# Performance work log

Measured on AMD Instinct MI355X. Metric: run time of the kernel, lower is better.

The kernel has to match this reference:

```python
import jax, jax.numpy as jnp
import numpy as np
from jax import lax

L = 12        # transformer layers
H = 768       # d_model
NH = 12       # heads
HD = H // NH  # head dim
F = 2048      # ffn dim (torch TransformerEncoderLayer default)
V = 128       # vocab_size (level logits)
NLV = 128     # n_levels (rows of routed weight W)
B, S = 8, 512
EPS = 1e-5


def _layer_norm(x, g, b):
    mu = jnp.mean(x, axis=-1, keepdims=True)
    var = jnp.mean(jnp.square(x - mu), axis=-1, keepdims=True)
    return g * (x - mu) / jnp.sqrt(var + EPS) + b


def _encoder(x, layer_params):
    # torch nn.TransformerEncoderLayer, post-LN, ReLU, eval mode (no dropout)
    def block(h, p):
        Wqkv, bqkv, Wo, bo, g1, bb1, W1, b1f, W2, b2f, g2, bb2 = p
        qkv = h @ Wqkv.T + bqkv                      # [B,S,3H]
        q, k, v = jnp.split(qkv, 3, axis=-1)
        sh = (h.shape[0], h.shape[1], NH, HD)
        q, k, v = q.reshape(sh), k.reshape(sh), v.reshape(sh)
        scores = jnp.einsum('bqhd,bkhd->bhqk', q, k) / jnp.sqrt(jnp.asarray(HD, h.dtype))
        attn = jax.nn.softmax(scores, axis=-1)
        o = jnp.einsum('bhqk,bkhd->bqhd', attn, v).reshape(h.shape)
        o = o @ Wo.T + bo
        h = _layer_norm(h + o, g1, bb1)
        f = jnp.maximum(h @ W1.T + b1f, 0.0) @ W2.T + b2f
        h = _layer_norm(h + f, g2, bb2)
        return h, None
    x, _ = lax.scan(block, x, layer_params)
    return x


def setup_inputs() -> dict:
    key = jax.random.key(0)
    ks = jax.random.split(key, 20)
    s = 0.02
    rn = lambda k, shp: jax.random.normal(k, shp, jnp.float32) * s
    inp = {
        'level_ids': jax.random.randint(ks[0], (B, S), 0, V, jnp.int32),
        'sublevel_ids': jax.random.randint(ks[1], (B, S), 0, V, jnp.int32),
        'bin_emb': rn(ks[2], (V, H)),
        'sub_emb': rn(ks[3], (V, H)),
        'Wqkv': rn(ks[4], (L, 3 * H, H)),
        'bqkv': jnp.zeros((L, 3 * H), jnp.float32),
        'Wo': rn(ks[5], (L, H, H)),
        'bo': jnp.zeros((L, H), jnp.float32),
        'ln1_g': jnp.ones((L, H), jnp.float32),
        'ln1_b': jnp.zeros((L, H), jnp.float32),
        'W1': rn(ks[6], (L, F, H)),
        'b1': jnp.zeros((L, F), jnp.float32),
        'W2': rn(ks[7], (L, H, F)),
        'b2': jnp.zeros((L, H), jnp.float32),
        'ln2_g': jnp.ones((L, H), jnp.float32),
        'ln2_b': jnp.zeros((L, H), jnp.float32),
        'W_lm': rn(ks[8], (V, H)),
        'b_lm': jnp.zeros((V,), jnp.float32),
        'W': rn(ks[9], (NLV, H, V)),       # routed per-level weights
        'bias': jnp.zeros((NLV, V), jnp.float32),
    }
    return inp


def reference(level_ids, sublevel_ids, bin_emb, sub_emb, Wqkv, bqkv, Wo, bo,
              ln1_g, ln1_b, W1, b1, W2, b2, ln2_g, ln2_b, W_lm, b_lm, W, bias):
    # embedding: sum of two id tables (tabular bin/subbin embedding)
    x = bin_emb[level_ids] + sub_emb[sublevel_ids]            # [B,S,H]
    layer_params = (Wqkv, bqkv, Wo, bo, ln1_g, ln1_b, W1, b1, W2, b2, ln2_g, ln2_b)
    x = _encoder(x, layer_params)                              # [B,S,H]
    out = x @ W_lm.T + b_lm                                    # [B,S,V]
    ix = jnp.argmax(out, axis=-1)                              # [B,S] routing index
    # per-token weight gather + batched vec-mat: the irregular hot path
    Wg = W[ix]                                                 # [B,S,H,V]
    sublevel_out = jnp.einsum('bsh,bshv->bsv', x, Wg) + bias[ix]
    return (out, sublevel_out)
```

## Files before the change

### kernel.cpp

```cpp
#include <hip/hip_runtime.h>
#include <cstdint>
#include <cstddef>

#define TOK 4096
#define HD_ 64
#define NH_ 12
#define H_ 768
#define F_ 2048
#define V_ 128
#define L_ 12
#define SEQ 512
#define BQKV (3*H_)
#define BATCH 8

typedef _Float16 f16;
typedef _Float16 f16x8 __attribute__((ext_vector_type(8)));
typedef _Float16 f16x4 __attribute__((ext_vector_type(4)));
typedef float    f32x4 __attribute__((ext_vector_type(4)));

#define GLDS16(g, l) __builtin_amdgcn_global_load_lds( \
    (const __attribute__((address_space(1))) uint32_t*)(g), \
    (__attribute__((address_space(3))) uint32_t*)(l), 16, 0, 0)

__device__ __forceinline__ float wave_sum(float v) {
#pragma unroll
  for (int m = 32; m >= 1; m >>= 1) v += __shfl_xor(v, m);
  return v;
}

__device__ __forceinline__ void split16(float v, f16& h, f16& lo) {
  h = (f16)v;
  lo = (f16)((v - (float)h) * 2048.0f);
}

__device__ __forceinline__ int swz(int r, int c) {
  int byte = (r << 7) + (c << 1);
  byte ^= (r & 7) << 4;
  return byte >> 1;
}

__global__ __launch_bounds__(256)
void k_convert(const float* __restrict__ src, f16* __restrict__ h, f16* __restrict__ l,
               int n4, float scale) {
  int i = blockIdx.x * 256 + threadIdx.x;
  int stride = gridDim.x * 256;
  for (; i < n4; i += stride) {
    float4 v = ((const float4*)src)[i];
    v.x *= scale; v.y *= scale; v.z *= scale; v.w *= scale;
    f16x4 vh, vl;
    f16 a, b;
    split16(v.x, a, b); vh[0] = a; vl[0] = b;
    split16(v.y, a, b); vh[1] = a; vl[1] = b;
    split16(v.z, a, b); vh[2] = a; vl[2] = b;
    split16(v.w, a, b); vh[3] = a; vl[3] = b;
    ((f16x4*)h)[i] = vh;
    ((f16x4*)l)[i] = vl;
  }
}

__global__ __launch_bounds__(256)
void k_embed2(const int* __restrict__ lid, const int* __restrict__ sid,
              const float* __restrict__ be, const float* __restrict__ se,
              float* __restrict__ x, f16* __restrict__ xh, f16* __restrict__ xl,
              int* __restrict__ counts) {
  int t = blockIdx.x;
  if (t == 0 && threadIdx.x < V_) counts[threadIdx.x] = 0;
  int li = lid[t], si = sid[t];
  const float* bp = be + (size_t)li * H_;
  const float* sp = se + (size_t)si * H_;
  size_t base = (size_t)t * H_;
#pragma unroll
  for (int j = 0; j < 3; ++j) {
    int hh = threadIdx.x + 256 * j;
    float v = bp[hh] + sp[hh];
    x[base + hh] = v;
    f16 a, b; split16(v, a, b);
    xh[base + hh] = a; xl[base + hh] = b;
  }
}

template<int BM, int BN, int MODE, int SPLIT>
__global__ __launch_bounds__(256, 2)
void k_gemm5(const f16* __restrict__ Ah, const f16* __restrict__ Al,
             const f16* __restrict__ Bh, const f16* __restrict__ Bl,
             const float* __restrict__ bias, float* __restrict__ C,
             f16* __restrict__ Ch, f16* __restrict__ Cl,
             int N, int K) {
  constexpr int MI = BM / 32, NJ = BN / 32;
  constexpr int IA = BM / 64, IB = BN / 64;
  constexpr int ABYT = BM * 64, BBYT = BN * 64;
  constexpr int BUFB = 2 * ABYT + 2 * BBYT;
  constexpr int NGL = 2 * (IA + IB);
  __shared__ __align__(16) char sm_[2 * BUFB];
  const int tid = threadIdx.x;
  const int lane = tid & 63, wid = tid >> 6;
  const int wr = wid >> 1, wc = wid & 1;

  const unsigned flat = blockIdx.x + gridDim.x * (blockIdx.y + gridDim.y * blockIdx.z);
  const unsigned G = gridDim.x >> 3;
  const unsigned xcd = flat & 7u;
  const unsigned idx = flat >> 3;
  const unsigned mt = xcd * G + idx % G;
  const unsigned rest = idx / G;
  const unsigned nt = rest % gridDim.y;
  const unsigned zt = rest / gridDim.y;

  const int bm = mt * BM, bn = nt * BN;
  const size_t rs = (size_t)K * 2;
  const size_t koff = (size_t)zt * (size_t)(K / SPLIT) * 2;

  const int srow = tid >> 2, schk = tid & 3;
  const char* ga[2][IA];
  const char* gb[2][IB];
#pragma unroll
  for (int u = 0; u < IA; ++u) {
    int row = u * 64 + srow;
    int c = schk ^ ((row >> 1) & 3);
    ga[0][u] = (const char*)Ah + (size_t)(bm + row) * rs + c * 16 + koff;
    ga[1][u] = (const char*)Al + (size_t)(bm + row) * rs + c * 16 + koff;
  }
#pragma unroll
  for (int u = 0; u < IB; ++u) {
    int row = u * 64 + srow;
    int c = schk ^ ((row >> 1) & 3);
    gb[0][u] = (const char*)Bh + (size_t)(bn + row) * rs + c * 16 + koff;
    gb[1][u] = (const char*)Bl + (size_t)(bn + row) * rs + c * 16 + koff;
  }

  const int rr = lane & 15, cgrp = lane >> 4;
  int aoff[MI][2], boff[NJ][2];
#pragma unroll
  for (int i = 0; i < MI; ++i) {
    int row = wr * (BM / 2) + i * 16 + rr;
    int sw = (cgrp ^ ((row >> 1) & 3)) * 16;
    aoff[i][0] = row * 64 + sw;
    aoff[i][1] = ABYT + row * 64 + sw;
  }
#pragma unroll
  for (int j = 0; j < NJ; ++j) {
    int row = wc * (BN / 2) + j * 16 + rr;
    int sw = (cgrp ^ ((row >> 1) & 3)) * 16;
    boff[j][0] = 2 * ABYT + row * 64 + sw;
    boff[j][1] = 2 * ABYT + BBYT + row * 64 + sw;
  }

  f32x4 aH[MI][NJ], aM[MI][NJ];
#pragma unroll
  for (int i = 0; i < MI; ++i)
#pragma unroll
    for (int j = 0; j < NJ; ++j)
#pragma unroll
      for (int q = 0; q < 4; ++q) { aH[i][j][q] = 0.0f; aM[i][j][q] = 0.0f; }

  auto STG = [&](char* bufbase) __attribute__((always_inline)) {
    char* base = bufbase + wid * 1024;
#pragma unroll
    for (int u = 0; u < IA; ++u) {
      GLDS16(ga[0][u], base + u * 4096);
      GLDS16(ga[1][u], base + ABYT + u * 4096);
      ga[0][u] += 64; ga[1][u] += 64;
    }
#pragma unroll
    for (int u = 0; u < IB; ++u) {
      GLDS16(gb[0][u], base + 2 * ABYT + u * 4096);
      GLDS16(gb[1][u], base + 2 * ABYT + BBYT + u * 4096);
      gb[0][u] += 64; gb[1][u] += 64;
    }
  };

  char* b0 = sm_;
  char* b1 = sm_ + BUFB;
  const int nst = (K / SPLIT) / 32;
  STG(b0);
  STG(b1);
  for (int s = 0; s < nst; ++s) {
    if (s < nst - 1) {
      asm volatile("s_waitcnt vmcnt(%0)" :: "i"(NGL) : "memory");
    } else {
      asm volatile("s_waitcnt vmcnt(0)" ::: "memory");
    }
    __builtin_amdgcn_s_barrier();
    __builtin_amdgcn_sched_barrier(0);
    const char* base = (s & 1) ? b1 : b0;
    f16x8 fb[NJ][2], fa[MI][2];
#pragma unroll
    for (int j = 0; j < NJ; ++j) {
      fb[j][0] = *(const f16x8*)(base + boff[j][0]);
      fb[j][1] = *(const f16x8*)(base + boff[j][1]);
    }
#pragma unroll
    for (int i = 0; i < MI; ++i) {
      fa[i][0] = *(const f16x8*)(base + aoff[i][0]);
      fa[i][1] = *(const f16x8*)(base + aoff[i][1]);
    }
    asm volatile("s_waitcnt lgkmcnt(0)" ::: "memory");
    __builtin_amdgcn_s_barrier();
    __builtin_amdgcn_sched_barrier(0);
    if (s + 2 < nst) STG((char*)base);
    __builtin_amdgcn_s_setprio(1);
#pragma unroll
    for (int i = 0; i < MI; ++i) {
#pragma unroll
      for (int j = 0; j < NJ; ++j) {
        aH[i][j] = __builtin_amdgcn_mfma_f32_16x16x32_f16(fa[i][0], fb[j][0], aH[i][j], 0, 0, 0);
        aM[i][j] = __builtin_amdgcn_mfma_f32_16x16x32_f16(fa[i][0], fb[j][1], aM[i][j], 0, 0, 0);
        aM[i][j] = __builtin_amdgcn_mfma_f32_16x16x32_f16(fa[i][1], fb[j][0], aM[i][j], 0, 0, 0);
      }
    }
    __builtin_amdgcn_s_setprio(0);
  }

  const int r4 = (lane >> 4) * 4, cc = lane & 15;
  float* Cp = (MODE == 3) ? (C + (size_t)zt * ((size_t)TOK * N)) : C;
#pragma unroll
  for (int i = 0; i < MI; ++i) {
#pragma unroll
    for (int j = 0; j < NJ; ++j) {
      int col = bn + wc * (BN / 2) + j * 16 + cc;
      float bz = (MODE == 3) ? 0.0f : bias[col];
#pragma unroll
      for (int q = 0; q < 4; ++q) {
        int row = bm + wr * (BM / 2) + i * 16 + r4 + q;
        float v = (aH[i][j][q] + aM[i][j][q] * (1.0f / 2048.0f)) * (1.0f / 64.0f) + bz;
        if (MODE == 0 || MODE == 3) {
          Cp[(size_t)row * N + col] = v;
        } else {
          if (MODE == 1) v = fmaxf(v, 0.0f);
          f16 a, b; split16(v, a, b);
          Ch[(size_t)row * N + col] = a;
          Cl[(size_t)row * N + col] = b;
        }
      }
    }
  }
}

__global__ __launch_bounds__(256)
void k_flash_mfma(const f16* __restrict__ ph, const f16* __restrict__ pl,
                  f16* __restrict__ oh, f16* __restrict__ ol) {
  __shared__ __align__(16) f16 VtH[4096];
  __shared__ __align__(16) f16 VtL[4096];
  __shared__ __align__(16) f16 PH[4096];
  __shared__ __align__(16) f16 PL[4096];
  __shared__ float PS[2][64];
  const int tid = threadIdx.x;
  const int lane = tid & 63, wid = tid >> 6;
  const int wr = wid >> 1, wc = wid & 1;
  const unsigned flat = blockIdx.x + 8u * blockIdx.y;
  const unsigned xcd = flat & 7u;
  const unsigned idx = flat >> 3;
  const int qt = idx & 7;
  const int bh = xcd * 12 + (idx >> 3);
  const int b = bh / NH_, hd = bh % NH_;
  const int rr = lane & 15, kg = (lane >> 4) * 8;
  const size_t tok0 = (size_t)b * SEQ;

  f16x8 qfh[2][2], qfl[2][2];
#pragma unroll
  for (int ifr = 0; ifr < 2; ++ifr)
#pragma unroll
    for (int ks = 0; ks < 2; ++ks) {
      size_t g = (tok0 + qt * 64 + wr * 32 + ifr * 16 + rr) * (size_t)BQKV + hd * HD_ + ks * 32 + kg;
      qfh[ifr][ks] = *(const f16x8*)&ph[g];
      qfl[ifr][ks] = *(const f16x8*)&pl[g];
    }

  f32x4 oha[2][2], oma[2][2];
  f32x4 ps[2];
#pragma unroll
  for (int i = 0; i < 2; ++i) {
#pragma unroll
    for (int q = 0; q < 4; ++q) ps[i][q] = 0.0f;
#pragma unroll
    for (int j = 0; j < 2; ++j)
#pragma unroll
      for (int q = 0; q < 4; ++q) { oha[i][j][q] = 0.0f; oma[i][j][q] = 0.0f; }
  }

  const int vj = tid >> 2;
  const int vs = tid & 3;

  for (int kt = 0; kt < SEQ / 64; ++kt) {
    __syncthreads();
#pragma unroll
    for (int s = 0; s < 2; ++s) {
      int d0 = (vs + s * 4) * 8;
      size_t g = (tok0 + kt * 64 + vj) * (size_t)BQKV + 2 * H_ + hd * HD_ + d0;
      f16x8 vh8 = *(const f16x8*)&ph[g];
      f16x8 vl8 = *(const f16x8*)&pl[g];
#pragma unroll
      for (int u = 0; u < 8; ++u) {
        VtH[swz(d0 + u, vj)] = vh8[u];
        VtL[swz(d0 + u, vj)] = vl8[u];
      }
    }
    __syncthreads();
    f16x8 kfh[2][2], kfl[2][2];
#pragma unroll
    for (int jf = 0; jf < 2; ++jf)
#pragma unroll
      for (int ks = 0; ks < 2; ++ks) {
        size_t g = (tok0 + kt * 64 + wc * 32 + jf * 16 + rr) * (size_t)BQKV + H_ + hd * HD_ + ks * 32 + kg;
        kfh[jf][ks] = *(const f16x8*)&ph[g];
        kfl[jf][ks] = *(const f16x8*)&pl[g];
      }
    f32x4 sh[2][2], sm2[2][2];
#pragma unroll
    for (int i = 0; i < 2; ++i)
#pragma unroll
      for (int j = 0; j < 2; ++j)
#pragma unroll
        for (int q = 0; q < 4; ++q) { sh[i][j][q] = 0.0f; sm2[i][j][q] = 0.0f; }
#pragma unroll
    for (int ifr = 0; ifr < 2; ++ifr)
#pragma unroll
      for (int jf = 0; jf < 2; ++jf)
#pragma unroll
        for (int ks = 0; ks < 2; ++ks) {
          sh[ifr][jf] = __builtin_amdgcn_mfma_f32_16x16x32_f16(qfh[ifr][ks], kfh[jf][ks], sh[ifr][jf], 0, 0, 0);
          sm2[ifr][jf] = __builtin_amdgcn_mfma_f32_16x16x32_f16(qfh[ifr][ks], kfl[jf][ks], sm2[ifr][jf], 0, 0, 0);
          sm2[ifr][jf] = __builtin_amdgcn_mfma_f32_16x16x32_f16(qfl[ifr][ks], kfh[jf][ks], sm2[ifr][jf], 0, 0, 0);
        }
#pragma unroll
    for (int ifr = 0; ifr < 2; ++ifr)
#pragma unroll
      for (int jf = 0; jf < 2; ++jf) {
        int pj = wc * 32 + jf * 16 + rr;
#pragma unroll
        for (int q = 0; q < 4; ++q) {
          int pi = wr * 32 + ifr * 16 + (lane >> 4) * 4 + q;
          float sval = (sh[ifr][jf][q] + sm2[ifr][jf][q] * (1.0f / 2048.0f)) * 0.125f;
          float p = expf(sval);
          ps[ifr][q] += p;
          f16 a, b2; split16(p, a, b2);
          PH[swz(pi, pj)] = a;
          PL[swz(pi, pj)] = b2;
        }
      }
    __syncthreads();
#pragma unroll
    for (int ks = 0; ks < 2; ++ks) {
      f16x8 pfh[2], pfl[2], vfh[2], vfl[2];
#pragma unroll
      for (int ifr = 0; ifr < 2; ++ifr) {
        pfh[ifr] = *(const f16x8*)&PH[swz(wr * 32 + ifr * 16 + rr, ks * 32 + kg)];
        pfl[ifr] = *(const f16x8*)&PL[swz(wr * 32 + ifr * 16 + rr, ks * 32 + kg)];
      }
#pragma unroll
      for (int jf = 0; jf < 2; ++jf) {
        vfh[jf] = *(const f16x8*)&VtH[swz(wc * 32 + jf * 16 + rr, ks * 32 + kg)];
        vfl[jf] = *(const f16x8*)&VtL[swz(wc * 32 + jf * 16 + rr, ks * 32 + kg)];
      }
#pragma unroll
      for (int ifr = 0; ifr < 2; ++ifr)
#pragma unroll
        for (int jf = 0; jf < 2; ++jf) {
          oha[ifr][jf] = __builtin_amdgcn_mfma_f32_16x16x32_f16(pfh[ifr], vfh[jf], oha[ifr][jf], 0, 0, 0);
          oma[ifr][jf] = __builtin_amdgcn_mfma_f32_16x16x32_f16(pfh[ifr], vfl[jf], oma[ifr][jf], 0, 0, 0);
          oma[ifr][jf] = __builtin_amdgcn_mfma_f32_16x16x32_f16(pfl[ifr], vfh[jf], oma[ifr][jf], 0, 0, 0);
        }
    }
  }

#pragma unroll
  for (int ifr = 0; ifr < 2; ++ifr)
#pragma unroll
    for (int m = 1; m < 16; m <<= 1)
#pragma unroll
      for (int q = 0; q < 4; ++q) ps[ifr][q] += __shfl_xor(ps[ifr][q], m);
  if (rr == 0) {
#pragma unroll
    for (int ifr = 0; ifr < 2; ++ifr)
#pragma unroll
      for (int q = 0; q < 4; ++q)
        PS[wc][wr * 32 + ifr * 16 + (lane >> 4) * 4 + q] = ps[ifr][q];
  }
  __syncthreads();

#pragma unroll
  for (int ifr = 0; ifr < 2; ++ifr)
#pragma unroll
    for (int jf = 0; jf < 2; ++jf)
#pragma unroll
      for (int q = 0; q < 4; ++q) {
        int i = wr * 32 + ifr * 16 + (lane >> 4) * 4 + q;
        float inv = 1.0f / (PS[0][i] + PS[1][i]);
        float o = (oha[ifr][jf][q] + oma[ifr][jf][q] * (1.0f / 2048.0f)) * inv;
        size_t g = (tok0 + qt * 64 + i) * (size_t)H_ + hd * HD_ + wc * 32 + jf * 16 + rr;
        f16 a, b2; split16(o, a, b2);
        oh[g] = a; ol[g] = b2;
      }
}

__global__ __launch_bounds__(256)
void k_ln_res3(const float* __restrict__ xin, const float* __restrict__ part,
               const float* __restrict__ bcol,
               const float* __restrict__ g, const float* __restrict__ bb,
               float* __restrict__ xout, f16* __restrict__ xh, f16* __restrict__ xl) {
  __shared__ float red[8];
  int t = blockIdx.x;
  const float* xr = xin + (size_t)t * H_;
  const float* p0 = part + (size_t)t * H_;
  const float* p1 = part + (size_t)TOK * H_ + (size_t)t * H_;
  float v[3];
#pragma unroll
  for (int j = 0; j < 3; ++j) {
    int hh = threadIdx.x + 256 * j;
    v[j] = xr[hh] + ((p0[hh] + p1[hh]) + bcol[hh]);
  }
  float s = v[0] + v[1] + v[2];
  s = wave_sum(s);
  int w = threadIdx.x >> 6;
  if ((threadIdx.x & 63) == 0) red[w] = s;
  __syncthreads();
  float mu = (red[0] + red[1] + red[2] + red[3]) * (1.0f / 768.0f);
  float q = 0.f;
#pragma unroll
  for (int j = 0; j < 3; ++j) { float d = v[j] - mu; q = fmaf(d, d, q); }
  q = wave_sum(q);
  if ((threadIdx.x & 63) == 0) red[4 + w] = q;
  __syncthreads();
  float var = (red[4] + red[5] + red[6] + red[7]) * (1.0f / 768.0f);
  float rinv = 1.0f / sqrtf(var + 1e-5f);
#pragma unroll
  for (int j = 0; j < 3; ++j) {
    int hh = threadIdx.x + 256 * j;
    float val = fmaf(g[hh], (v[j] - mu) * rinv, bb[hh]);
    size_t idx = (size_t)t * H_ + hh;
    xout[idx] = val;
    f16 a, b; split16(val, a, b);
    xh[idx] = a; xl[idx] = b;
  }
}

__global__ __launch_bounds__(64)
void k_argmax2(const float* __restrict__ part, const float* __restrict__ blm,
               float* __restrict__ out0, int* __restrict__ ix,
               int* __restrict__ counts) {
  int t = blockIdx.x, l = threadIdx.x;
  const size_t S = (size_t)TOK * V_;
  size_t c0 = (size_t)t * V_ + l;
  size_t c1 = c0 + 64;
  float v0 = ((part[c0] + part[S + c0]) + part[2 * S + c0]) + part[3 * S + c0] + blm[l];
  float v1 = ((part[c1] + part[S + c1]) + part[2 * S + c1]) + part[3 * S + c1] + blm[l + 64];
  out0[c0] = v0;
  out0[c1] = v1;
  float best = v0; int bi = l;
  if (v1 > best) { best = v1; bi = 64 + l; }
#pragma unroll
  for (int m = 1; m < 64; m <<= 1) {
    float ov = __shfl_xor(best, m);
    int oi = __shfl_xor(bi, m);
    if (ov > best || (ov == best && oi < bi)) { best = ov; bi = oi; }
  }
  if (l == 0) { ix[t] = bi; atomicAdd(&counts[bi], 1); }
}

__global__ __launch_bounds__(128)
void k_prep(const int* __restrict__ counts, int* __restrict__ offsets,
            int* __restrict__ cursors, int4* __restrict__ chunks,
            int* __restrict__ nchunks) {
  __shared__ int s[128];
  int r = threadIdx.x;
  int c = counts[r];
  s[r] = c; __syncthreads();
  for (int d = 1; d < 128; d <<= 1) {
    int v = (r >= d) ? s[r - d] : 0; __syncthreads();
    s[r] += v; __syncthreads();
  }
  int off = s[r] - c;
  offsets[r] = off;
  cursors[r] = 0;
  int nch = (c + 15) >> 4;
  __syncthreads();
  s[r] = nch; __syncthreads();
  for (int d = 1; d < 128; d <<= 1) {
    int v = (r >= d) ? s[r - d] : 0; __syncthreads();
    s[r] += v; __syncthreads();
  }
  int cb = s[r] - nch;
  for (int u = 0; u < nch; ++u) {
    int rem = c - u * 16;
    chunks[cb + u] = make_int4(r, off + u * 16, rem < 16 ? rem : 16, 0);
  }
  if (r == 127) *nchunks = s[127];
}

__global__ __launch_bounds__(256)
void k_scatter(const int* __restrict__ ix, const int* __restrict__ offsets,
               int* __restrict__ cursors, int* __restrict__ bucket) {
  int t = blockIdx.x * 256 + threadIdx.x;
  int r = ix[t];
  int p = atomicAdd(&cursors[r], 1);
  bucket[offsets[r] + p] = t;
}

__global__ __launch_bounds__(256)
void k_convT(const float* __restrict__ W, f16* __restrict__ wth, f16* __restrict__ wtl) {
  __shared__ float tile[64][65];
  const int r = blockIdx.x, vb = blockIdx.y * 64;
  const int tid = threadIdx.x;
  const int la = tid & 63, wv = tid >> 6;
  for (int ht = 0; ht < H_ / 64; ++ht) {
    int h0 = ht * 64;
#pragma unroll
    for (int i = 0; i < 16; ++i) {
      int row = wv + i * 4;
      tile[row][la] = W[(size_t)r * (H_ * V_) + (size_t)(h0 + row) * V_ + vb + la];
    }
    __syncthreads();
#pragma unroll
    for (int i = 0; i < 16; ++i) {
      int vl = wv + i * 4;
      float w = tile[la][vl];
      f16 a, b; split16(w, a, b);
      size_t o = ((size_t)r * V_ + vb + vl) * H_ + h0 + la;
      wth[o] = a; wtl[o] = b;
    }
    __syncthreads();
  }
}

__global__ __launch_bounds__(256)
void k_sublevel3(const f16* __restrict__ xh, const f16* __restrict__ xl,
                 const f16* __restrict__ wth, const f16* __restrict__ wtl,
                 const float* __restrict__ bias, const int* __restrict__ bucket,
                 const int4* __restrict__ chunks, const int* __restrict__ nchunks,
                 float* __restrict__ out) {
  int c = blockIdx.x;
  if (c >= *nchunks) return;
  int4 ch = chunks[c];
  int r = ch.x, ts = ch.y, nt = ch.z;
  __shared__ int toks[16];
  int tid = threadIdx.x;
  if (tid < 16) toks[tid] = bucket[ts + (tid < nt ? tid : 0)];
  __syncthreads();
  const int lane = tid & 63, wid = tid >> 6;
  const int rr = lane & 15, kg = (lane >> 4) * 8;
  const int myTok = toks[rr];
  const size_t abase = (size_t)myTok * H_ + kg;

  f32x4 aH[2], aM[2];
#pragma unroll
  for (int j = 0; j < 2; ++j)
#pragma unroll
    for (int q = 0; q < 4; ++q) { aH[j][q] = 0.0f; aM[j][q] = 0.0f; }

  size_t wb[2];
#pragma unroll
  for (int j = 0; j < 2; ++j)
    wb[j] = ((size_t)r * V_ + wid * 32 + j * 16 + rr) * H_ + kg;

  for (int k0 = 0; k0 < H_; k0 += 32) {
    f16x8 ah = *(const f16x8*)&xh[abase + k0];
    f16x8 al = *(const f16x8*)&xl[abase + k0];
#pragma unroll
    for (int j = 0; j < 2; ++j) {
      f16x8 bh = *(const f16x8*)&wth[wb[j] + k0];
      f16x8 bl = *(const f16x8*)&wtl[wb[j] + k0];
      aH[j] = __builtin_amdgcn_mfma_f32_16x16x32_f16(ah, bh, aH[j], 0, 0, 0);
      aM[j] = __builtin_amdgcn_mfma_f32_16x16x32_f16(ah, bl, aM[j], 0, 0, 0);
      aM[j] = __builtin_amdgcn_mfma_f32_16x16x32_f16(al, bh, aM[j], 0, 0, 0);
    }
  }

  const int r4 = (lane >> 4) * 4, cc = lane & 15;
#pragma unroll
  for (int j = 0; j < 2; ++j) {
#pragma unroll
    for (int q = 0; q < 4; ++q) {
      int row = r4 + q;
      if (row < nt) {
        int col = wid * 32 + j * 16 + cc;
        out[(size_t)toks[row] * V_ + col] =
            aH[j][q] + aM[j][q] * (1.0f / 2048.0f) + bias[(size_t)r * V_ + col];
      }
    }
  }
}

extern "C" void kernel_launch(void* const* d_in, const int* in_sizes, int n_in,
                              void* d_out, int out_size, void* d_ws, size_t ws_size,
                              hipStream_t stream) {
  const int*   lid  = (const int*)d_in[0];
  const int*   sid  = (const int*)d_in[1];
  const float* be   = (const float*)d_in[2];
  const float* se   = (const float*)d_in[3];
  const float* Wqkv = (const float*)d_in[4];
  const float* bqkv = (const float*)d_in[5];
  const float* Wo   = (const float*)d_in[6];
  const float* bo   = (const float*)d_in[7];
  const float* g1   = (const float*)d_in[8];
  const float* b1n  = (const float*)d_in[9];
  const float* W1   = (const float*)d_in[10];
  const float* b1f  = (const float*)d_in[11];
  const float* W2   = (const float*)d_in[12];
  const float* b2f  = (const float*)d_in[13];
  const float* g2   = (const float*)d_in[14];
  const float* b2n  = (const float*)d_in[15];
  const float* Wlm  = (const float*)d_in[16];
  const float* blm  = (const float*)d_in[17];
  const float* Wrt  = (const float*)d_in[18];
  const float* brt  = (const float*)d_in[19];

  char* ws = (char*)d_ws;
  float* x    = (float*)(ws + 0);
  f16*   xh   = (f16*)  (ws + 12582912);
  f16*   xl   = (f16*)  (ws + 18874368);
  f16*   qh   = (f16*)  (ws + 25165824);
  f16*   ql   = (f16*)  (ws + 44040192);
  f16*   midh = qh;
  f16*   midl = ql;
  f16*   ath  = (f16*)  (ws + 62914560);
  f16*   atl  = (f16*)  (ws + 69206016);
  float* bufY = (float*)(ws + 75497472);
  float* pO   = (float*)(ws + 25165824);
  float* pF   = (float*)(ws + 62914560);
  float* pLM  = bufY;
  f16*   wth  = (f16*)  (ws + 25165824);
  f16*   wtl  = (f16*)  (ws + 50331648);
  f16*   wsh  = (f16*)  (ws + 88080384);
  f16*   wsl  = (f16*)  (ws + 91619328);
  f16*   wlmh = (f16*)  (ws + 95158272);
  f16*   wlml = (f16*)  (ws + 95354880);
  int*   ix   = (int*)  (ws + 95551488);
  int*   counts  = (int*)(ws + 95567872);
  int*   cursors = (int*)(ws + 95568384);
  int*   offsets = (int*)(ws + 95568896);
  int4*  chunks  = (int4*)(ws + 95569920);
  int*   nchunks = (int*)(ws + 95576064);
  int*   bucket  = (int*)(ws + 95576320);
  const size_t need = 95592704;
  if (ws_size < need) return;

  bool big = ws_size >= 95600640ull + 265000000ull;
  f16 *bWqh = nullptr, *bWql = nullptr, *bWoh = nullptr, *bWol = nullptr,
      *bW1h = nullptr, *bW1l = nullptr, *bW2h = nullptr, *bW2l = nullptr;
  if (big) {
    char* p = ws + 95600640;
    bWqh = (f16*)p; p += 42467328;
    bWql = (f16*)p; p += 42467328;
    bWoh = (f16*)p; p += 14155776;
    bWol = (f16*)p; p += 14155776;
    bW1h = (f16*)p; p += 37748736;
    bW1l = (f16*)p; p += 37748736;
    bW2h = (f16*)p; p += 37748736;
    bW2l = (f16*)p; p += 37748736;
    k_convert<<<2048, 256, 0, stream>>>(Wqkv, bWqh, bWql, L_ * BQKV * H_ / 4, 64.f);
    k_convert<<<2048, 256, 0, stream>>>(Wo,   bWoh, bWol, L_ * H_ * H_ / 4, 64.f);
    k_convert<<<2048, 256, 0, stream>>>(W1,   bW1h, bW1l, L_ * F_ * H_ / 4, 64.f);
    k_convert<<<2048, 256, 0, stream>>>(W2,   bW2h, bW2l, L_ * H_ * F_ / 4, 64.f);
  }
  k_convert<<<96, 256, 0, stream>>>(Wlm, wlmh, wlml, V_ * H_ / 4, 64.f);

  float* out0 = (float*)d_out;
  float* out1 = out0 + (size_t)TOK * V_;

  k_embed2<<<TOK, 256, 0, stream>>>(lid, sid, be, se, x, xh, xl, counts);

  for (int l = 0; l < L_; ++l) {
    const float* bqkv_l = bqkv + (size_t)l * BQKV;
    const float* bo_l   = bo   + (size_t)l * H_;
    const float* g1_l   = g1   + (size_t)l * H_;
    const float* b1n_l  = b1n  + (size_t)l * H_;
    const float* b1f_l  = b1f  + (size_t)l * F_;
    const float* b2f_l  = b2f  + (size_t)l * H_;
    const float* g2_l   = g2   + (size_t)l * H_;
    const float* b2n_l  = b2n  + (size_t)l * H_;

    const f16 *wh, *wl2;
    if (big) { wh = bWqh + (size_t)l * BQKV * H_; wl2 = bWql + (size_t)l * BQKV * H_; }
    else {
      k_convert<<<1728, 256, 0, stream>>>(Wqkv + (size_t)l * BQKV * H_, wsh, wsl, BQKV * H_ / 4, 64.f);
      wh = wsh; wl2 = wsl;
    }
    k_gemm5<128, 128, 2, 1><<<dim3(TOK / 128, BQKV / 128, 1), 256, 0, stream>>>(
        xh, xl, wh, wl2, bqkv_l, nullptr, qh, ql, BQKV, H_);
    k_flash_mfma<<<dim3(SEQ / 64, BATCH * NH_), 256, 0, stream>>>(qh, ql, ath, atl);
    if (big) { wh = bWoh + (size_t)l * H_ * H_; wl2 = bWol + (size_t)l * H_ * H_; }
    else {
      k_convert<<<576, 256, 0, stream>>>(Wo + (size_t)l * H_ * H_, wsh, wsl, H_ * H_ / 4, 64.f);
      wh = wsh; wl2 = wsl;
    }
    k_gemm5<128, 128, 3, 2><<<dim3(TOK / 128, H_ / 128, 2), 256, 0, stream>>>(
        ath, atl, wh, wl2, nullptr, pO, nullptr, nullptr, H_, H_);
    k_ln_res3<<<TOK, 256, 0, stream>>>(x, pO, bo_l, g1_l, b1n_l, x, xh, xl);
    if (big) { wh = bW1h + (size_t)l * F_ * H_; wl2 = bW1l + (size_t)l * F_ * H_; }
    else {
      k_convert<<<1536, 256, 0, stream>>>(W1 + (size_t)l * F_ * H_, wsh, wsl, F_ * H_ / 4, 64.f);
      wh = wsh; wl2 = wsl;
    }
    k_gemm5<128, 128, 1, 1><<<dim3(TOK / 128, F_ / 128, 1), 256, 0, stream>>>(
        xh, xl, wh, wl2, b1f_l, nullptr, midh, midl, F_, H_);
    if (big) { wh = bW2h + (size_t)l * H_ * F_; wl2 = bW2l + (size_t)l * H_ * F_; }
    else {
      k_convert<<<1536, 256, 0, stream>>>(W2 + (size_t)l * H_ * F_, wsh, wsl, H_ * F_ / 4, 64.f);
      wh = wsh; wl2 = wsl;
    }
    k_gemm5<128, 128, 3, 2><<<dim3(TOK / 128, H_ / 128, 2), 256, 0, stream>>>(
        midh, midl, wh, wl2, nullptr, pF, nullptr, nullptr, H_, F_);
    k_ln_res3<<<TOK, 256, 0, stream>>>(x, pF, b2f_l, g2_l, b2n_l, x, xh, xl);
  }

  k_gemm5<64, 64, 3, 4><<<dim3(TOK / 64, V_ / 64, 4), 256, 0, stream>>>(
      xh, xl, wlmh, wlml, nullptr, pLM, nullptr, nullptr, V_, H_);
  k_convT<<<dim3(V_, 2), 256, 0, stream>>>(Wrt, wth, wtl);
  k_argmax2<<<TOK, 64, 0, stream>>>(pLM, blm, out0, ix, counts);
  k_prep<<<1, 128, 0, stream>>>(counts, offsets, cursors, chunks, nchunks);
  k_scatter<<<TOK / 256, 256, 0, stream>>>(ix, offsets, cursors, bucket);
  k_sublevel3<<<384, 256, 0, stream>>>(xh, xl, wth, wtl, brt, bucket, chunks, nchunks, out1);
}
```

Baseline: 3.278 ms.

## Write V transposed from QKV GEMM epilogue and read it directly in attention

The QKV GEMM gains a mode that stores the V section in a per-head transposed [b,h,d,s] layout, so the attention kernel no longer stages and transposes V through shared memory each key tile. The score MFMA operands are swapped so each lane holds four consecutive keys, letting P be written to LDS as vector stores and simplifying the row-sum reduction. This removes a scalar LDS transpose and a barrier per tile, but the GEMM epilogue now does strided, uncoalesced scalar stores for V, and V fragments are loaded straight from global memory.

Result: slower. 3.696 ms (+12.7%).

```diff
diff --git a/kernel.cpp b/kernel.cpp
--- a/kernel.cpp
+++ b/kernel.cpp
@@ -85,6 +85,7 @@
              const f16* __restrict__ Bh, const f16* __restrict__ Bl,
              const float* __restrict__ bias, float* __restrict__ C,
              f16* __restrict__ Ch, f16* __restrict__ Cl,
+             f16* __restrict__ Vh, f16* __restrict__ Vl,
              int N, int K) {
   constexpr int MI = BM / 32, NJ = BN / 32;
   constexpr int IA = BM / 64, IB = BN / 64;
@@ -224,6 +225,18 @@
         float v = (aH[i][j][q] + aM[i][j][q] * (1.0f / 2048.0f)) * (1.0f / 64.0f) + bz;
         if (MODE == 0 || MODE == 3) {
           Cp[(size_t)row * N + col] = v;
+        } else if (MODE == 4) {
+          f16 a, b; split16(v, a, b);
+          if (col < 2 * H_) {
+            Ch[(size_t)row * N + col] = a;
+            Cl[(size_t)row * N + col] = b;
+          } else {
+            int d = col & 63;
+            int hd2 = (col - 2 * H_) >> 6;
+            int bb = row >> 9, ss = row & 511;
+            size_t o = (((size_t)(bb * NH_ + hd2)) * HD_ + d) * SEQ + ss;
+            Vh[o] = a; Vl[o] = b;
+          }
         } else {
           if (MODE == 1) v = fmaxf(v, 0.0f);
           f16 a, b; split16(v, a, b);
@@ -236,10 +249,9 @@
 }
 
 __global__ __launch_bounds__(256)
-void k_flash_mfma(const f16* __restrict__ ph, const f16* __restrict__ pl,
-                  f16* __restrict__ oh, f16* __restrict__ ol) {
-  __shared__ __align__(16) f16 VtH[4096];
-  __shared__ __align__(16) f16 VtL[4096];
+void k_flash2(const f16* __restrict__ ph, const f16* __restrict__ pl,
+              const f16* __restrict__ vth, const f16* __restrict__ vtl,
+              f16* __restrict__ oh, f16* __restrict__ ol) {
   __shared__ __align__(16) f16 PH[4096];
   __shared__ __align__(16) f16 PL[4096];
   __shared__ float PS[2][64];
@@ -254,6 +266,7 @@
   const int b = bh / NH_, hd = bh % NH_;
   const int rr = lane & 15, kg = (lane >> 4) * 8;
   const size_t tok0 = (size_t)b * SEQ;
+  const size_t vbase = (size_t)bh * HD_ * SEQ;
 
   f16x8 qfh[2][2], qfl[2][2];
 #pragma unroll
@@ -266,35 +279,15 @@
     }
 
   f32x4 oha[2][2], oma[2][2];
-  f32x4 ps[2];
-#pragma unroll
-  for (int i = 0; i < 2; ++i) {
-#pragma unroll
-    for (int q = 0; q < 4; ++q) ps[i][q] = 0.0f;
+  float psum[2] = {0.f, 0.f};
+#pragma unroll
+  for (int i = 0; i < 2; ++i)
 #pragma unroll
     for (int j = 0; j < 2; ++j)
 #pragma unroll
       for (int q = 0; q < 4; ++q) { oha[i][j][q] = 0.0f; oma[i][j][q] = 0.0f; }
-  }
-
-  const int vj = tid >> 2;
-  const int vs = tid & 3;
 
   for (int kt = 0; kt < SEQ / 64; ++kt) {
-    __syncthreads();
-#pragma unroll
-    for (int s = 0; s < 2; ++s) {
-      int d0 = (vs + s * 4) * 8;
-      size_t g = (tok0 + kt * 64 + vj) * (size_t)BQKV + 2 * H_ + hd * HD_ + d0;
-      f16x8 vh8 = *(const f16x8*)&ph[g];
-      f16x8 vl8 = *(const f16x8*)&pl[g];
-#pragma unroll
-      for (int u = 0; u < 8; ++u) {
-        VtH[swz(d0 + u, vj)] = vh8[u];
-        VtL[swz(d0 + u, vj)] = vl8[u];
-      }
-    }
-    __syncthreads();
     f16x8 kfh[2][2], kfl[2][2];
 #pragma unroll
     for (int jf = 0; jf < 2; ++jf)
@@ -306,37 +299,41 @@
       }
     f32x4 sh[2][2], sm2[2][2];
 #pragma unroll
-    for (int i = 0; i < 2; ++i)
-#pragma unroll
-      for (int j = 0; j < 2; ++j)
-#pragma unroll
-        for (int q = 0; q < 4; ++q) { sh[i][j][q] = 0.0f; sm2[i][j][q] = 0.0f; }
-#pragma unroll
-    for (int ifr = 0; ifr < 2; ++ifr)
-#pragma unroll
-      for (int jf = 0; jf < 2; ++jf)
+    for (int j = 0; j < 2; ++j)
+#pragma unroll
+      for (int i = 0; i < 2; ++i)
+#pragma unroll
+        for (int q = 0; q < 4; ++q) { sh[j][i][q] = 0.0f; sm2[j][i][q] = 0.0f; }
+#pragma unroll
+    for (int jf = 0; jf < 2; ++jf)
+#pragma unroll
+      for (int ifr = 0; ifr < 2; ++ifr)
 #pragma unroll
         for (int ks = 0; ks < 2; ++ks) {
-          sh[ifr][jf] = __builtin_amdgcn_mfma_f32_16x16x32_f16(qfh[ifr][ks], kfh[jf][ks], sh[ifr][jf], 0, 0, 0);
-          sm2[ifr][jf] = __builtin_amdgcn_mfma_f32_16x16x32_f16(qfh[ifr][ks], kfl[jf][ks], sm2[ifr][jf], 0, 0, 0);
-          sm2[ifr][jf] = __builtin_amdgcn_mfma_f32_16x16x32_f16(qfl[ifr][ks], kfh[jf][ks], sm2[ifr][jf], 0, 0, 0);
+          sh[jf][ifr]  = __builtin_amdgcn_mfma_f32_16x16x32_f16(kfh[jf][ks], qfh[ifr][ks], sh[jf][ifr], 0, 0, 0);
+          sm2[jf][ifr] = __builtin_amdgcn_mfma_f32_16x16x32_f16(kfl[jf][ks], qfh[ifr][ks], sm2[jf][ifr], 0, 0, 0);
+          sm2[jf][ifr] = __builtin_amdgcn_mfma_f32_16x16x32_f16(kfh[jf][ks], qfl[ifr][ks], sm2[jf][ifr], 0, 0, 0);
         }
-#pragma unroll
-    for (int ifr = 0; ifr < 2; ++ifr)
+    __syncthreads();
+#pragma unroll
+    for (int ifr = 0; ifr < 2; ++ifr) {
 #pragma unroll
       for (int jf = 0; jf < 2; ++jf) {
-        int pj = wc * 32 + jf * 16 + rr;
+        f16x4 v4h, v4l;
 #pragma unroll
         for (int q = 0; q < 4; ++q) {
-          int pi = wr * 32 + ifr * 16 + (lane >> 4) * 4 + q;
-          float sval = (sh[ifr][jf][q] + sm2[ifr][jf][q] * (1.0f / 2048.0f)) * 0.125f;
+          float sval = (sh[jf][ifr][q] + sm2[jf][ifr][q] * (1.0f / 2048.0f)) * 0.125f;
           float p = expf(sval);
-          ps[ifr][q] += p;
+          psum[ifr] += p;
           f16 a, b2; split16(p, a, b2);
-          PH[swz(pi, pj)] = a;
-          PL[swz(pi, pj)] = b2;
+          v4h[q] = a; v4l[q] = b2;
         }
+        int qi = wr * 32 + ifr * 16 + rr;
+        int j0 = wc * 32 + jf * 16 + (lane >> 4) * 4;
+        *(f16x4*)&PH[swz(qi, j0)] = v4h;
+        *(f16x4*)&PL[swz(qi, j0)] = v4l;
       }
+    }
     __syncthreads();
 #pragma unroll
     for (int ks = 0; ks < 2; ++ks) {
@@ -348,8 +345,9 @@
       }
 #pragma unroll
       for (int jf = 0; jf < 2; ++jf) {
-        vfh[jf] = *(const f16x8*)&VtH[swz(wc * 32 + jf * 16 + rr, ks * 32 + kg)];
-        vfl[jf] = *(const f16x8*)&VtL[swz(wc * 32 + jf * 16 + rr, ks * 32 + kg)];
+        size_t g = vbase + (size_t)(wc * 32 + jf * 16 + rr) * SEQ + kt * 64 + ks * 32 + kg;
+        vfh[jf] = *(const f16x8*)&vth[g];
+        vfl[jf] = *(const f16x8*)&vtl[g];
       }
 #pragma unroll
       for (int ifr = 0; ifr < 2; ++ifr)
@@ -363,17 +361,13 @@
   }
 
 #pragma unroll
-  for (int ifr = 0; ifr < 2; ++ifr)
-#pragma unroll
-    for (int m = 1; m < 16; m <<= 1)
-#pragma unroll
-      for (int q = 0; q < 4; ++q) ps[ifr][q] += __shfl_xor(ps[ifr][q], m);
-  if (rr == 0) {
-#pragma unroll
-    for (int ifr = 0; ifr < 2; ++ifr)
-#pragma unroll
-      for (int q = 0; q < 4; ++q)
-        PS[wc][wr * 32 + ifr * 16 + (lane >> 4) * 4 + q] = ps[ifr][q];
+  for (int ifr = 0; ifr < 2; ++ifr) {
+    psum[ifr] += __shfl_xor(psum[ifr], 16);
+    psum[ifr] += __shfl_xor(psum[ifr], 32);
+  }
+  if (lane < 16) {
+    PS[wc][wr * 32 + lane]      = psum[0];
+    PS[wc][wr * 32 + 16 + lane] = psum[1];
   }
   __syncthreads();
 
@@ -614,6 +608,8 @@
   f16*   ath  = (f16*)  (ws + 62914560);
   f16*   atl  = (f16*)  (ws + 69206016);
   float* bufY = (float*)(ws + 75497472);
+  f16*   vth  = (f16*)  (ws + 75497472);
+  f16*   vtl  = (f16*)  (ws + 81788928);
   float* pO   = (float*)(ws + 25165824);
   float* pF   = (float*)(ws + 62914560);
   float* pLM  = bufY;
@@ -674,16 +670,16 @@
       k_convert<<<1728, 256, 0, stream>>>(Wqkv + (size_t)l * BQKV * H_, wsh, wsl, BQKV * H_ / 4, 64.f);
       wh = wsh; wl2 = wsl;
     }
-    k_gemm5<128, 128, 2, 1><<<dim3(TOK / 128, BQKV / 128, 1), 256, 0, stream>>>(
-        xh, xl, wh, wl2, bqkv_l, nullptr, qh, ql, BQKV, H_);
-    k_flash_mfma<<<dim3(SEQ / 64, BATCH * NH_), 256, 0, stream>>>(qh, ql, ath, atl);
+    k_gemm5<128, 128, 4, 1><<<dim3(TOK / 128, BQKV / 128, 1), 256, 0, stream>>>(
+        xh, xl, wh, wl2, bqkv_l, nullptr, qh, ql, vth, vtl, BQKV, H_);
+    k_flash2<<<dim3(SEQ / 64, BATCH * NH_), 256, 0, stream>>>(qh, ql, vth, vtl, ath, atl);
     if (big) { wh = bWoh + (size_t)l * H_ * H_; wl2 = bWol + (size_t)l * H_ * H_; }
     else {
       k_convert<<<576, 256, 0, stream>>>(Wo + (size_t)l * H_ * H_, wsh, wsl, H_ * H_ / 4, 64.f);
       wh = wsh; wl2 = wsl;
     }
     k_gemm5<128, 128, 3, 2><<<dim3(TOK / 128, H_ / 128, 2), 256, 0, stream>>>(
-        ath, atl, wh, wl2, nullptr, pO, nullptr, nullptr, H_, H_);
+        ath, atl, wh, wl2, nullptr, pO, nullptr, nullptr, nullptr, nullptr, H_, H_);
     k_ln_res3<<<TOK, 256, 0, stream>>>(x, pO, bo_l, g1_l, b1n_l, x, xh, xl);
     if (big) { wh = bW1h + (size_t)l * F_ * H_; wl2 = bW1l + (size_t)l * F_ * H_; }
     else {
@@ -691,19 +687,19 @@
       wh = wsh; wl2 = wsl;
     }
     k_gemm5<128, 128, 1, 1><<<dim3(TOK / 128, F_ / 128, 1), 256, 0, stream>>>(
-        xh, xl, wh, wl2, b1f_l, nullptr, midh, midl, F_, H_);
+        xh, xl, wh, wl2, b1f_l, nullptr, midh, midl, nullptr, nullptr, F_, H_);
     if (big) { wh = bW2h + (size_t)l * H_ * F_; wl2 = bW2l + (size_t)l * H_ * F_; }
     else {
       k_convert<<<1536, 256, 0, stream>>>(W2 + (size_t)l * H_ * F_, wsh, wsl, H_ * F_ / 4, 64.f);
       wh = wsh; wl2 = wsl;
     }
     k_gemm5<128, 128, 3, 2><<<dim3(TOK / 128, H_ / 128, 2), 256, 0, stream>>>(
-        midh, midl, wh, wl2, nullptr, pF, nullptr, nullptr, H_, F_);
+        midh, midl, wh, wl2, nullptr, pF, nullptr, nullptr, nullptr, nullptr, H_, F_);
     k_ln_res3<<<TOK, 256, 0, stream>>>(x, pF, b2f_l, g2_l, b2n_l, x, xh, xl);
   }
 
   k_gemm5<64, 64, 3, 4><<<dim3(TOK / 64, V_ / 64, 4), 256, 0, stream>>>(
-      xh, xl, wlmh, wlml, nullptr, pLM, nullptr, nullptr, V_, H_);
+      xh, xl, wlmh, wlml, nullptr, pLM, nullptr, nullptr, nullptr, nullptr, V_, H_);
   k_convT<<<dim3(V_, 2), 256, 0, stream>>>(Wrt, wth, wtl);
   k_argmax2<<<TOK, 64, 0, stream>>>(pLM, blm, out0, ix, counts);
   k_prep<<<1, 128, 0, stream>>>(counts, offsets, cursors, chunks, nchunks);
```
